# Optimization experiments

Hardware: AMD Instinct MI355X
Metric: run time of the kernel (lower is better)

## Reference

```python
import jax, jax.numpy as jnp
import numpy as np

N = 50000      # nodes
E = 800000     # edges (before self loops)
IN = 128       # in_channels
H = 4          # heads
C = 32         # hidden_channels (per head)
D = H * C      # concat output dim = 128
NEG_SLOPE = 0.2
LN_EPS = 1e-5


def setup_inputs() -> dict:
    key = jax.random.key(0)
    ks = jax.random.split(key, 24)
    def p(k, shape, s=0.1):
        return jax.random.normal(k, shape, dtype=jnp.float32) * s
    inp = {
        "x": p(ks[0], (N, IN), 1.0),
        "edge_index": jax.random.randint(ks[1], (2, E), 0, N, dtype=jnp.int32),
    }
    i = 2
    for l, ind in [(0, IN), (1, D)]:
        inp[f"Wl{l}"] = p(ks[i], (ind, D)); i += 1
        inp[f"bl{l}"] = p(ks[i], (D,), 0.02); i += 1
        inp[f"Wr{l}"] = p(ks[i], (ind, D)); i += 1
        inp[f"br{l}"] = p(ks[i], (D,), 0.02); i += 1
        inp[f"att{l}"] = p(ks[i], (H, C)); i += 1
        inp[f"Wres{l}"] = p(ks[i], (ind, D)); i += 1
        inp[f"bias{l}"] = p(ks[i], (D,), 0.02); i += 1
        inp[f"g{l}"] = jnp.ones((D,), jnp.float32)
        inp[f"be{l}"] = jnp.zeros((D,), jnp.float32)
    return inp


def _gatv2_layer(x, src, dst, Wl, bl, Wr, br, att, Wres, bias):
    """GATv2Conv with concat heads, add_self_loops already applied, residual."""
    n = x.shape[0]
    xl = (x @ Wl + bl).reshape(n, H, C)   # source transform
    xr = (x @ Wr + br).reshape(n, H, C)   # target transform
    # edge-level attention logits: e = a . LeakyReLU(xl[j] + xr[i])  [E, H]
    eh = jax.nn.leaky_relu(xl[src] + xr[dst], negative_slope=NEG_SLOPE)  # [E,H,C]
    score = jnp.einsum('ehc,hc->eh', eh, att)                            # [E,H]
    # segment softmax over incoming edges of each destination node
    smax = jax.ops.segment_max(score, dst, num_segments=n)               # [N,H]
    ex = jnp.exp(score - smax[dst])
    ssum = jax.ops.segment_sum(ex, dst, num_segments=n)                  # [N,H]
    alpha = ex / ssum[dst]                                               # [E,H]
    msg = xl[src] * alpha[:, :, None]                                    # [E,H,C]
    out = jax.ops.segment_sum(msg, dst, num_segments=n).reshape(n, D)
    return out + x @ Wres + bias  # residual (bias=False linear) + final bias


def _layernorm_relu(x, g, b):
    mu = jnp.mean(x, axis=-1, keepdims=True)
    var = jnp.mean(jnp.square(x - mu), axis=-1, keepdims=True)
    return jax.nn.relu((x - mu) * jax.lax.rsqrt(var + LN_EPS) * g + b)


def reference(x, edge_index,
              Wl0, bl0, Wr0, br0, att0, Wres0, bias0, g0, be0,
              Wl1, bl1, Wr1, br1, att1, Wres1, bias1, g1, be1):
    n = x.shape[0]
    loops = jnp.arange(n, dtype=edge_index.dtype)
    src = jnp.concatenate([edge_index[0], loops])  # add_self_loops=True
    dst = jnp.concatenate([edge_index[1], loops])
    h = _gatv2_layer(x, src, dst, Wl0, bl0, Wr0, br0, att0, Wres0, bias0)
    h = _layernorm_relu(h, g0, be0)
    h = _gatv2_layer(h, src, dst, Wl1, bl1, Wr1, br1, att1, Wres1, bias1)
    h = _layernorm_relu(h, g1, be1)
    return h
```

## Files before the change

kernel.cpp:

```cpp
#include <hip/hip_runtime.h>
#include <math.h>

#define D 128
#define LRELU 0.2f
#define LN_EPS 1e-5f
#define INV_LN2 1.4426950408889634f

#define NBMAX 512
#define CAP 4096
#define P1CHUNK 8192

typedef __attribute__((ext_vector_type(8))) short short8;
typedef __attribute__((ext_vector_type(8))) unsigned short ushort8;
typedef __attribute__((ext_vector_type(4))) float f32x4;
typedef __attribute__((ext_vector_type(2))) float f32x2;
typedef __attribute__((ext_vector_type(2))) unsigned int u32x2;
typedef __attribute__((ext_vector_type(4))) unsigned int u32x4;

static __device__ __forceinline__ unsigned short f2bf(float f) {
    union { float f; unsigned u; } a; a.f = f;
    unsigned r = a.u + 0x7FFFu + ((a.u >> 16) & 1u);
    return (unsigned short)(r >> 16);
}

static __device__ __forceinline__ f32x2 pk_add(f32x2 a, f32x2 b) {
    f32x2 d; asm("v_pk_add_f32 %0, %1, %2" : "=v"(d) : "v"(a), "v"(b)); return d;
}
static __device__ __forceinline__ f32x2 pk_mul(f32x2 a, f32x2 b) {
    f32x2 d; asm("v_pk_mul_f32 %0, %1, %2" : "=v"(d) : "v"(a), "v"(b)); return d;
}
static __device__ __forceinline__ f32x2 pk_fma(f32x2 a, f32x2 b, f32x2 c) {
    f32x2 d; asm("v_pk_fma_f32 %0, %1, %2, %3" : "=v"(d) : "v"(a), "v"(b), "v"(c)); return d;
}
static __device__ __forceinline__ f32x2 pk_abs(f32x2 a) {
    u32x2 u = __builtin_bit_cast(u32x2, a);
    u &= 0x7FFFFFFFu;
    return __builtin_bit_cast(f32x2, u);
}
static __device__ __forceinline__ f32x2 bf2x(unsigned u) {
    f32x2 r;
    r.x = __uint_as_float(u << 16);
    r.y = __uint_as_float(u & 0xFFFF0000u);
    return r;
}

static __device__ __forceinline__ float red4_dpp(float p) {
    int v = __builtin_amdgcn_update_dpp(0, __builtin_bit_cast(int, p), 0xB1, 0xf, 0xf, true);
    p += __builtin_bit_cast(float, v);
    v = __builtin_amdgcn_update_dpp(0, __builtin_bit_cast(int, p), 0x4E, 0xf, 0xf, true);
    p += __builtin_bit_cast(float, v);
    return p;
}

#define SCB 256


__global__ __launch_bounds__(256) void k_prep(
    const int* __restrict__ srcp, const int* __restrict__ dstp,
    int* __restrict__ bcur, unsigned* __restrict__ ebuf, int E, int N,
    const float* __restrict__ X, ushort* __restrict__ Xb, int Mp,
    const float* __restrict__ W0, const float* __restrict__ W1, const float* __restrict__ W2,
    const float* __restrict__ W3, const float* __restrict__ W4, const float* __restrict__ W5,
    ushort* __restrict__ Wp, int nP1, int nCV)
{
    const int bx = blockIdx.x;
    const int tid = threadIdx.x;
    if (bx < nP1) {
        __shared__ int h[NBMAX];
        const int E2 = E + N;
        const int e0 = bx * P1CHUNK;
        const int e1 = min(e0 + P1CHUNK, E2);
        for (int t = tid; t < NBMAX; t += 256) h[t] = 0;
        __syncthreads();
        for (int e = e0 + tid; e < e1; e += 256) {
            int d = (e < E) ? dstp[e] : e - E;
            atomicAdd(&h[d >> 7], 1);
        }
        __syncthreads();
        for (int b = tid; b < NBMAX; b += 256) {
            int c = h[b];
            h[b] = c ? atomicAdd(&bcur[b], c) : 0;
        }
        __syncthreads();
        for (int e = e0 + tid; e < e1; e += 256) {
            int d  = (e < E) ? dstp[e] : e - E;
            int sc = (e < E) ? srcp[e] : e - E;
            int b = d >> 7;
            int pos = atomicAdd(&h[b], 1) & (CAP - 1);
            ebuf[(size_t)b * CAP + pos] = ((unsigned)sc << 7) | (unsigned)(d & 127);
        }
    } else if (bx < nP1 + nCV) {
        int idx = (bx - nP1) * 256 + tid;
        if (idx >= Mp * (D / 4)) return;
        ushort4 o;
        if (idx < N * (D / 4)) {
            float4 v = ((const float4*)X)[idx];
            o.x = f2bf(v.x); o.y = f2bf(v.y); o.z = f2bf(v.z); o.w = f2bf(v.w);
        } else {
            o = make_ushort4(0, 0, 0, 0);
        }
        ((ushort4*)Xb)[idx] = o;
    } else {
        int bid = bx - nP1 - nCV;
        int m = bid >> 6;
        int o = ((bid & 63) << 8) + tid;
        const float* W;
        if (m == 0) W = W0; else if (m == 1) W = W1; else if (m == 2) W = W2;
        else if (m == 3) W = W3; else if (m == 4) W = W4; else W = W5;
        int j  = o & 7;
        int l  = (o >> 3) & 63;
        int ct = (o >> 9) & 7;
        int kc = o >> 12;
        int k   = kc * 32 + ((l >> 4) << 3) + j;
        int col = (ct << 4) + (l & 15);
        Wp[m * 16384 + o] = f2bf(W[k * D + col]);
    }
}


__global__ __launch_bounds__(256) void bhist_kernel(const unsigned* __restrict__ ebuf,
                                                    const int* __restrict__ bcur,
                                                    int* __restrict__ deg,
                                                    int* __restrict__ btot, int N) {
    const int b = blockIdx.x;
    const int base = b << 7;
    const int tid = threadIdx.x;
    __shared__ int h[128];
    __shared__ int t2[2];
    if (tid < 128) h[tid] = 0;
    __syncthreads();
    const int cnt = min(bcur[b], CAP);
    for (int k = tid; k < cnt; k += 256) {
        unsigned v = ebuf[(size_t)b * CAP + k];
        atomicAdd(&h[v & 127], 1);
    }
    __syncthreads();
    int v = (tid < 128) ? h[tid] : 0;
    if (tid < 128 && base + tid < N) deg[base + tid] = v;
    #pragma unroll
    for (int o = 32; o >= 1; o >>= 1) v += __shfl_xor(v, o);
    if (tid == 0)  t2[0] = v;
    if (tid == 64) t2[1] = v;
    __syncthreads();
    if (tid == 0) btot[b] = t2[0] + t2[1];
}


static __device__ __forceinline__ void gemm_body(
    int bxg, int seg, int tid,
    const ushort* __restrict__ Xb, const ushort* __restrict__ Wp,
    const float* __restrict__ bl, const float* __restrict__ br,
    ushort* __restrict__ XLb, ushort* __restrict__ XRb, float* __restrict__ RES)
{
    const int l = tid & 63;
    const int wave = tid >> 6;
    const int wr = wave >> 1, wc = wave & 1;
    const int brow = bxg * 128 + wr * 64;
    const ushort* W = Wp + seg * 16384;

    f32x4 acc[4][4] = {};
    const int arow = brow + (l & 15);
    const int koff = (l >> 4) * 8;

    #pragma unroll
    for (int kc = 0; kc < 4; ++kc) {
        short8 A[4], B[4];
        #pragma unroll
        for (int at = 0; at < 4; ++at)
            A[at] = *(const short8*)&Xb[(size_t)(arow + at * 16) * D + kc * 32 + koff];
        #pragma unroll
        for (int ct = 0; ct < 4; ++ct) {
            int ctg = wc * 4 + ct;
            B[ct] = *(const short8*)&W[(((kc * 8 + ctg) * 64) + l) * 8];
        }
        #pragma unroll
        for (int at = 0; at < 4; ++at)
            #pragma unroll
            for (int ct = 0; ct < 4; ++ct)
                acc[at][ct] = __builtin_amdgcn_mfma_f32_16x16x32_bf16(A[at], B[ct], acc[at][ct], 0, 0, 0);
    }

    const int c = l & 15;
    const int r0 = (l >> 4) * 4;
    const float* bias = (seg == 0) ? bl : ((seg == 1) ? br : nullptr);
    #pragma unroll
    for (int ct = 0; ct < 4; ++ct) {
        int gcol = wc * 64 + ct * 16 + c;
        float bv = bias ? bias[gcol] : 0.f;
        #pragma unroll
        for (int at = 0; at < 4; ++at) {
            #pragma unroll
            for (int r = 0; r < 4; ++r) {
                int grow = brow + at * 16 + r0 + r;
                float v = acc[at][ct][r] + bv;
                size_t off = (size_t)grow * D + gcol;
                if (seg == 0)      XLb[off] = f2bf(v);
                else if (seg == 1) XRb[off] = f2bf(v);
                else               RES[off] = v;
            }
        }
    }
}


__global__ __launch_bounds__(256) void k_mid(
    const unsigned* __restrict__ ebuf, const int* __restrict__ bcur,
    const int* __restrict__ deg, const int* __restrict__ btot,
    int* __restrict__ off, int* __restrict__ csrc, int N, int NB, int nblk,
    const ushort* __restrict__ Xb, const ushort* __restrict__ Wp,
    const float* __restrict__ bl, const float* __restrict__ br,
    ushort* __restrict__ XLb, ushort* __restrict__ XRb, float* __restrict__ RES)
{
    const int bx = blockIdx.x;
    if (bx < NB) {
        const int b = bx;
        const int base = b << 7;
        const int tid = threadIdx.x;
        __shared__ int cur[128];
        __shared__ int wsum[4];
        __shared__ int wtot[2];

        int acc = 0;
        for (int t = tid; t < b; t += 256) acc += btot[t];
        #pragma unroll
        for (int o = 32; o >= 1; o >>= 1) acc += __shfl_xor(acc, o);
        if ((tid & 63) == 0) wsum[tid >> 6] = acc;
        __syncthreads();
        const int B = wsum[0] + wsum[1] + wsum[2] + wsum[3];

        int dv = 0;
        if (tid < 128 && base + tid < N) dv = deg[base + tid];
        int incl = dv;
        if (tid < 128) {
            #pragma unroll
            for (int o = 1; o < 64; o <<= 1) {
                int u = __shfl_up(incl, o);
                if ((tid & 63) >= o) incl += u;
            }
        }
        if (tid == 63)  wtot[0] = incl;
        if (tid == 127) wtot[1] = incl;
        __syncthreads();
        if (tid < 128) {
            int add = (tid >= 64) ? wtot[0] : 0;
            int excl = B + add + incl - dv;
            cur[tid] = excl;
            if (base + tid < N) off[base + tid] = excl;
        }
        if (b == NB - 1 && tid == 0) off[N] = B + wtot[0] + wtot[1];
        __syncthreads();

        const int cnt = min(bcur[b], CAP);
        for (int k = tid; k < cnt; k += 256) {
            unsigned v = ebuf[(size_t)b * CAP + k];
            int p = atomicAdd(&cur[v & 127], 1);
            csrc[p] = v >> 7;
        }
    } else {
        int bid = bx - NB;
        int seg = bid / nblk;
        int bxg = bid - seg * nblk;
        gemm_body(bxg, seg, threadIdx.x, Xb, Wp, bl, br, XLb, XRb, RES);
    }
}

__global__ __launch_bounds__(256) void gemm_mfma(
    const ushort* __restrict__ Xb, const ushort* __restrict__ Wp,
    const float* __restrict__ bl, const float* __restrict__ br,
    ushort* __restrict__ XLb, ushort* __restrict__ XRb, float* __restrict__ RES)
{
    gemm_body(blockIdx.x, blockIdx.y, threadIdx.x, Xb, Wp, bl, br, XLb, XRb, RES);
}


__global__ __launch_bounds__(256) void gat_node(
    const ushort* __restrict__ XLb, const ushort* __restrict__ XRb, const float* __restrict__ RES,
    const float* __restrict__ att, const float* __restrict__ bias,
    const float* __restrict__ g, const float* __restrict__ be,
    const int* __restrict__ off, const int* __restrict__ csrc,
    float* __restrict__ OUTf, ushort* __restrict__ OUTb)
{
    const int l = threadIdx.x & 63;
    const int i = blockIdx.x * 16 + (threadIdx.x >> 6) * 4 + (l >> 4);
    const int f = (l & 15) * 8;
    const unsigned ibase = ((unsigned)i << 7) + f;
    const int lb = l & 48;

    f32x2 at06[4], at04[4];
    #pragma unroll
    for (int k = 0; k < 4; ++k) {
        float2 a = *(const float2*)&att[f + k * 2];
        f32x2 av; av.x = a.x; av.y = a.y;
        at06[k] = av * (0.6f * INV_LN2);
        at04[k] = av * (0.4f * INV_LN2);
    }

    u32x4 xru = __builtin_nontemporal_load((const u32x4*)&XRb[ibase]);
    f32x2 xr2[4];
    xr2[0] = bf2x(xru.x); xr2[1] = bf2x(xru.y); xr2[2] = bf2x(xru.z); xr2[3] = bf2x(xru.w);

    const int e0 = off[i], e1 = off[i + 1];
    const int len = e1 - e0;
    int mx = max(len, __shfl_xor(len, 16));
    mx = max(mx, __shfl_xor(mx, 32));

    float m = -1e30f, s = 0.f;
    f32x2 a2[4] = {};

    for (int c0 = 0; c0 < mx; c0 += 16) {
        int myj = __builtin_nontemporal_load(&csrc[min(e0 + c0 + (l & 15), e1 - 1)]);
        const int rem = mx - c0;
        const int nbb = min(4, (rem + 3) >> 2);
        const int kleft = len - c0;

        u32x4 u_[4];
        {
            int s0 = __shfl(myj, lb + 0);
            int s1 = __shfl(myj, lb + 1);
            int s2 = __shfl(myj, lb + 2);
            int s3 = __shfl(myj, lb + 3);
            u_[0] = *(const u32x4*)&XLb[((unsigned)s0 << 7) + f];
            u_[1] = *(const u32x4*)&XLb[((unsigned)s1 << 7) + f];
            u_[2] = *(const u32x4*)&XLb[((unsigned)s2 << 7) + f];
            u_[3] = *(const u32x4*)&XLb[((unsigned)s3 << 7) + f];
        }

        #pragma unroll
        for (int bb = 0; bb < 4; ++bb) {
            if (bb >= nbb) break;
            u32x4 uc[4];
            #pragma unroll
            for (int j = 0; j < 4; ++j) uc[j] = u_[j];
            if (bb + 1 < nbb) {
                int s0 = __shfl(myj, lb + (bb + 1) * 4 + 0);
                int s1 = __shfl(myj, lb + (bb + 1) * 4 + 1);
                int s2 = __shfl(myj, lb + (bb + 1) * 4 + 2);
                int s3 = __shfl(myj, lb + (bb + 1) * 4 + 3);
                u_[0] = *(const u32x4*)&XLb[((unsigned)s0 << 7) + f];
                u_[1] = *(const u32x4*)&XLb[((unsigned)s1 << 7) + f];
                u_[2] = *(const u32x4*)&XLb[((unsigned)s2 << 7) + f];
                u_[3] = *(const u32x4*)&XLb[((unsigned)s3 << 7) + f];
            }

            const int kb = kleft - bb * 4;
            f32x2 xp[4][4];
            float p[4];
            #pragma unroll
            for (int j = 0; j < 4; ++j) {
                xp[j][0] = bf2x(uc[j].x);
                xp[j][1] = bf2x(uc[j].y);
                xp[j][2] = bf2x(uc[j].z);
                xp[j][3] = bf2x(uc[j].w);
                f32x2 v0 = pk_add(xp[j][0], xr2[0]);
                f32x2 pj2 = pk_mul(v0, at06[0]);
                pj2 = pk_fma(pk_abs(v0), at04[0], pj2);
                #pragma unroll
                for (int k = 1; k < 4; ++k) {
                    f32x2 v = pk_add(xp[j][k], xr2[k]);
                    pj2 = pk_fma(v, at06[k], pj2);
                    pj2 = pk_fma(pk_abs(v), at04[k], pj2);
                }
                float pj = pj2.x + pj2.y;
                pj = red4_dpp(pj);
                p[j] = (j < kb) ? pj : -1e30f;
            }
            float pmax = fmaxf(fmaxf(p[0], p[1]), fmaxf(p[2], p[3]));
            float nm = fmaxf(m, pmax);
            float so = exp2f(m - nm);
            float w0 = exp2f(p[0] - nm), w1 = exp2f(p[1] - nm);
            float w2 = exp2f(p[2] - nm), w3 = exp2f(p[3] - nm);
            s = s * so + ((w0 + w1) + (w2 + w3));
            f32x2 so2; so2.x = so; so2.y = so;
            f32x2 w02; w02.x = w0; w02.y = w0;
            f32x2 w12; w12.x = w1; w12.y = w1;
            f32x2 w22; w22.x = w2; w22.y = w2;
            f32x2 w32; w32.x = w3; w32.y = w3;
            #pragma unroll
            for (int k = 0; k < 4; ++k) {
                f32x2 t = pk_mul(xp[0][k], w02);
                t = pk_fma(xp[1][k], w12, t);
                t = pk_fma(xp[2][k], w22, t);
                t = pk_fma(xp[3][k], w32, t);
                a2[k] = pk_fma(a2[k], so2, t);
            }
            m = nm;
        }
    }

    const f32x4 rsA = __builtin_nontemporal_load((const f32x4*)&RES[ibase]);
    const f32x4 rsB = __builtin_nontemporal_load((const f32x4*)&RES[ibase + 4]);
    const float4 biA = *(const float4*)&bias[f];
    const float4 biB = *(const float4*)&bias[f + 4];
    float inv = 1.f / s;
    float r0 = a2[0].x * inv + rsA.x + biA.x;
    float r1 = a2[0].y * inv + rsA.y + biA.y;
    float r2 = a2[1].x * inv + rsA.z + biA.z;
    float r3 = a2[1].y * inv + rsA.w + biA.w;
    float r4 = a2[2].x * inv + rsB.x + biB.x;
    float r5 = a2[2].y * inv + rsB.y + biB.y;
    float r6 = a2[3].x * inv + rsB.z + biB.z;
    float r7 = a2[3].y * inv + rsB.w + biB.w;

    float sum = ((r0 + r1) + (r2 + r3)) + ((r4 + r5) + (r6 + r7));
    float sq  = ((r0 * r0 + r1 * r1) + (r2 * r2 + r3 * r3))
              + ((r4 * r4 + r5 * r5) + (r6 * r6 + r7 * r7));
    #pragma unroll
    for (int o = 8; o >= 1; o >>= 1) {
        sum += __shfl_xor(sum, o);
        sq  += __shfl_xor(sq, o);
    }
    float mu  = sum * (1.f / 128.f);
    float var = sq * (1.f / 128.f) - mu * mu;
    float isd = rsqrtf(var + LN_EPS);
    const float4 gvA = *(const float4*)&g[f];
    const float4 gvB = *(const float4*)&g[f + 4];
    const float4 bvA = *(const float4*)&be[f];
    const float4 bvB = *(const float4*)&be[f + 4];
    float o0 = fmaxf((r0 - mu) * isd * gvA.x + bvA.x, 0.f);
    float o1 = fmaxf((r1 - mu) * isd * gvA.y + bvA.y, 0.f);
    float o2 = fmaxf((r2 - mu) * isd * gvA.z + bvA.z, 0.f);
    float o3 = fmaxf((r3 - mu) * isd * gvA.w + bvA.w, 0.f);
    float o4 = fmaxf((r4 - mu) * isd * gvB.x + bvB.x, 0.f);
    float o5 = fmaxf((r5 - mu) * isd * gvB.y + bvB.y, 0.f);
    float o6 = fmaxf((r6 - mu) * isd * gvB.z + bvB.z, 0.f);
    float o7 = fmaxf((r7 - mu) * isd * gvB.w + bvB.w, 0.f);

    if (OUTb) {
        ushort8 ob;
        ob[0] = f2bf(o0); ob[1] = f2bf(o1); ob[2] = f2bf(o2); ob[3] = f2bf(o3);
        ob[4] = f2bf(o4); ob[5] = f2bf(o5); ob[6] = f2bf(o6); ob[7] = f2bf(o7);
        __builtin_nontemporal_store(ob, (ushort8*)&OUTb[ibase]);
    } else {
        f32x4 oA; oA.x = o0; oA.y = o1; oA.z = o2; oA.w = o3;
        f32x4 oB; oB.x = o4; oB.y = o5; oB.z = o6; oB.w = o7;
        __builtin_nontemporal_store(oA, (f32x4*)&OUTf[ibase]);
        __builtin_nontemporal_store(oB, (f32x4*)&OUTf[ibase + 4]);
    }
}


extern "C" void kernel_launch(void* const* d_in, const int* in_sizes, int n_in,
                              void* d_out, int out_size, void* d_ws, size_t ws_size,
                              hipStream_t stream)
{
    const float* x    = (const float*)d_in[0];
    const int*   ei   = (const int*)d_in[1];
    const float* Wl0  = (const float*)d_in[2];
    const float* bl0  = (const float*)d_in[3];
    const float* Wr0  = (const float*)d_in[4];
    const float* br0  = (const float*)d_in[5];
    const float* att0 = (const float*)d_in[6];
    const float* Wres0= (const float*)d_in[7];
    const float* bias0= (const float*)d_in[8];
    const float* g0   = (const float*)d_in[9];
    const float* be0  = (const float*)d_in[10];
    const float* Wl1  = (const float*)d_in[11];
    const float* bl1  = (const float*)d_in[12];
    const float* Wr1  = (const float*)d_in[13];
    const float* br1  = (const float*)d_in[14];
    const float* att1 = (const float*)d_in[15];
    const float* Wres1= (const float*)d_in[16];
    const float* bias1= (const float*)d_in[17];
    const float* g1   = (const float*)d_in[18];
    const float* be1  = (const float*)d_in[19];

    const int N  = in_sizes[0] / D;
    const int E  = in_sizes[1] / 2;
    const int E2 = E + N;
    const int nblk = (N + 127) / 128;
    const int Mp = nblk * 128;
    const int NB = nblk;

    char* w = (char*)d_ws;
    ushort* Xb  = (ushort*)w; w += (size_t)Mp * D * 2;
    ushort* Hb  = (ushort*)w; w += (size_t)Mp * D * 2;
    ushort* XLb = (ushort*)w; w += (size_t)Mp * D * 2;
    ushort* XRb = (ushort*)w; w += (size_t)Mp * D * 2;
    float*  RES = (float*)w;  w += (size_t)Mp * D * 4;
    ushort* Wp  = (ushort*)w; w += (size_t)6 * 16384 * 2;
    int* deg     = (int*)w; w += (size_t)N * 4;
    int* off     = (int*)w; w += (size_t)(N + 1) * 4;
    int* bcur    = (int*)w; w += (size_t)NBMAX * 4;
    int* btot    = (int*)w; w += (size_t)NBMAX * 4;
    unsigned* ebuf = (unsigned*)w; w += (size_t)NB * CAP * 4;
    int* csrc    = (int*)w; w += (size_t)E2 * 4;

    const int* srcp = ei;
    const int* dstp = ei + E;

    const int nP1 = (E2 + P1CHUNK - 1) / P1CHUNK;
    const int nCV = (Mp * (D / 4) + 255) / 256;
    const int nPW = 6 * 64;
    const int nGM = nblk * 3;

    hipMemsetAsync(bcur, 0, (size_t)NBMAX * 4, stream);
    k_prep<<<nP1 + nCV + nPW, 256, 0, stream>>>(srcp, dstp, bcur, ebuf, E, N,
                                                x, Xb, Mp,
                                                Wl0, Wr0, Wres0, Wl1, Wr1, Wres1,
                                                Wp, nP1, nCV);
    bhist_kernel<<<NB, 256, 0, stream>>>(ebuf, bcur, deg, btot, N);

    k_mid<<<NB + nGM, 256, 0, stream>>>(ebuf, bcur, deg, btot, off, csrc, N, NB, nblk,
                                        Xb, Wp, bl0, br0, XLb, XRb, RES);

    const int gatg = N / 16;
    dim3 ggrid(nblk, 3);

    gat_node<<<gatg, 256, 0, stream>>>(XLb, XRb, RES, att0, bias0, g0, be0, off, csrc, nullptr, Hb);
    gemm_mfma<<<ggrid, 256, 0, stream>>>(Hb, Wp + 3 * 16384, bl1, br1, XLb, XRb, RES);
    gat_node<<<gatg, 256, 0, stream>>>(XLb, XRb, RES, att1, bias1, g1, be1, off, csrc, (float*)d_out, nullptr);
}
```

Before: 186.4 us.

## Store residual in bf16 and split online softmax into two accumulator chains

The residual projection output is now written and read as bf16 instead of fp32, halving that buffer's write and read traffic in the GEMM and node kernels. The gat_node edge loop keeps two independent online-softmax states (max, sum, accumulators) that alternate per sub-batch and are merged at the end. This shortens the serial dependency through the rescale chain so more work can overlap. Weights past the valid count are now explicitly zeroed. The cost is extra registers, a branch per sub-batch, and lower precision in the residual term.

After: 185.1 us. About the same (-0.6%).

```diff
diff --git a/kernel.cpp b/kernel.cpp
--- a/kernel.cpp
+++ b/kernel.cpp
@@ -150,7 +150,7 @@
     int bxg, int seg, int tid,
     const ushort* __restrict__ Xb, const ushort* __restrict__ Wp,
     const float* __restrict__ bl, const float* __restrict__ br,
-    ushort* __restrict__ XLb, ushort* __restrict__ XRb, float* __restrict__ RES)
+    ushort* __restrict__ XLb, ushort* __restrict__ XRb, ushort* __restrict__ RESb)
 {
     const int l = tid & 63;
     const int wave = tid >> 6;
@@ -194,9 +194,9 @@
                 int grow = brow + at * 16 + r0 + r;
                 float v = acc[at][ct][r] + bv;
                 size_t off = (size_t)grow * D + gcol;
-                if (seg == 0)      XLb[off] = f2bf(v);
-                else if (seg == 1) XRb[off] = f2bf(v);
-                else               RES[off] = v;
+                if (seg == 0)      XLb[off]  = f2bf(v);
+                else if (seg == 1) XRb[off]  = f2bf(v);
+                else               RESb[off] = f2bf(v);
             }
         }
     }
@@ -209,7 +209,7 @@
     int* __restrict__ off, int* __restrict__ csrc, int N, int NB, int nblk,
     const ushort* __restrict__ Xb, const ushort* __restrict__ Wp,
     const float* __restrict__ bl, const float* __restrict__ br,
-    ushort* __restrict__ XLb, ushort* __restrict__ XRb, float* __restrict__ RES)
+    ushort* __restrict__ XLb, ushort* __restrict__ XRb, ushort* __restrict__ RESb)
 {
     const int bx = blockIdx.x;
     if (bx < NB) {
@@ -260,21 +260,21 @@
         int bid = bx - NB;
         int seg = bid / nblk;
         int bxg = bid - seg * nblk;
-        gemm_body(bxg, seg, threadIdx.x, Xb, Wp, bl, br, XLb, XRb, RES);
+        gemm_body(bxg, seg, threadIdx.x, Xb, Wp, bl, br, XLb, XRb, RESb);
     }
 }
 
 __global__ __launch_bounds__(256) void gemm_mfma(
     const ushort* __restrict__ Xb, const ushort* __restrict__ Wp,
     const float* __restrict__ bl, const float* __restrict__ br,
-    ushort* __restrict__ XLb, ushort* __restrict__ XRb, float* __restrict__ RES)
+    ushort* __restrict__ XLb, ushort* __restrict__ XRb, ushort* __restrict__ RESb)
 {
-    gemm_body(blockIdx.x, blockIdx.y, threadIdx.x, Xb, Wp, bl, br, XLb, XRb, RES);
+    gemm_body(blockIdx.x, blockIdx.y, threadIdx.x, Xb, Wp, bl, br, XLb, XRb, RESb);
 }
 
 
 __global__ __launch_bounds__(256) void gat_node(
-    const ushort* __restrict__ XLb, const ushort* __restrict__ XRb, const float* __restrict__ RES,
+    const ushort* __restrict__ XLb, const ushort* __restrict__ XRb, const ushort* __restrict__ RESb,
     const float* __restrict__ att, const float* __restrict__ bias,
     const float* __restrict__ g, const float* __restrict__ be,
     const int* __restrict__ off, const int* __restrict__ csrc,
@@ -304,8 +304,10 @@
     int mx = max(len, __shfl_xor(len, 16));
     mx = max(mx, __shfl_xor(mx, 32));
 
-    float m = -1e30f, s = 0.f;
-    f32x2 a2[4] = {};
+    float mA = -1e30f, sA = 0.f;
+    float mB = -1e30f, sB = 0.f;
+    f32x2 aA[4] = {};
+    f32x2 aB[4] = {};
 
     for (int c0 = 0; c0 < mx; c0 += 16) {
         int myj = __builtin_nontemporal_load(&csrc[min(e0 + c0 + (l & 15), e1 - 1)]);
@@ -364,42 +366,72 @@
                 pj = red4_dpp(pj);
                 p[j] = (j < kb) ? pj : -1e30f;
             }
+            float m0 = (bb & 1) ? mB : mA;
+            float s0v = (bb & 1) ? sB : sA;
             float pmax = fmaxf(fmaxf(p[0], p[1]), fmaxf(p[2], p[3]));
-            float nm = fmaxf(m, pmax);
-            float so = exp2f(m - nm);
+            float nm = fmaxf(m0, pmax);
+            float so = exp2f(m0 - nm);
             float w0 = exp2f(p[0] - nm), w1 = exp2f(p[1] - nm);
             float w2 = exp2f(p[2] - nm), w3 = exp2f(p[3] - nm);
-            s = s * so + ((w0 + w1) + (w2 + w3));
+            w0 = (0 < kb) ? w0 : 0.f;
+            w1 = (1 < kb) ? w1 : 0.f;
+            w2 = (2 < kb) ? w2 : 0.f;
+            w3 = (3 < kb) ? w3 : 0.f;
+            float sn = s0v * so + ((w0 + w1) + (w2 + w3));
             f32x2 so2; so2.x = so; so2.y = so;
             f32x2 w02; w02.x = w0; w02.y = w0;
             f32x2 w12; w12.x = w1; w12.y = w1;
             f32x2 w22; w22.x = w2; w22.y = w2;
             f32x2 w32; w32.x = w3; w32.y = w3;
-            #pragma unroll
-            for (int k = 0; k < 4; ++k) {
-                f32x2 t = pk_mul(xp[0][k], w02);
-                t = pk_fma(xp[1][k], w12, t);
-                t = pk_fma(xp[2][k], w22, t);
-                t = pk_fma(xp[3][k], w32, t);
-                a2[k] = pk_fma(a2[k], so2, t);
+            if (bb & 1) {
+                #pragma unroll
+                for (int k = 0; k < 4; ++k) {
+                    f32x2 t = pk_mul(xp[0][k], w02);
+                    t = pk_fma(xp[1][k], w12, t);
+                    t = pk_fma(xp[2][k], w22, t);
+                    t = pk_fma(xp[3][k], w32, t);
+                    aB[k] = pk_fma(aB[k], so2, t);
+                }
+                mB = nm; sB = sn;
+            } else {
+                #pragma unroll
+                for (int k = 0; k < 4; ++k) {
+                    f32x2 t = pk_mul(xp[0][k], w02);
+                    t = pk_fma(xp[1][k], w12, t);
+                    t = pk_fma(xp[2][k], w22, t);
+                    t = pk_fma(xp[3][k], w32, t);
+                    aA[k] = pk_fma(aA[k], so2, t);
+                }
+                mA = nm; sA = sn;
             }
-            m = nm;
-        }
-    }
-
-    const f32x4 rsA = __builtin_nontemporal_load((const f32x4*)&RES[ibase]);
-    const f32x4 rsB = __builtin_nontemporal_load((const f32x4*)&RES[ibase + 4]);
+        }
+    }
+
+    float nmv = fmaxf(mA, mB);
+    float soA = exp2f(mA - nmv);
+    float soB = exp2f(mB - nmv);
+    float s = sA * soA + sB * soB;
+    f32x2 soA2; soA2.x = soA; soA2.y = soA;
+    f32x2 soB2; soB2.x = soB; soB2.y = soB;
+    f32x2 a2[4];
+    #pragma unroll
+    for (int k = 0; k < 4; ++k)
+        a2[k] = pk_add(pk_mul(aA[k], soA2), pk_mul(aB[k], soB2));
+
+    u32x4 ru = __builtin_nontemporal_load((const u32x4*)&RESb[ibase]);
+    f32x2 rs2[4];
+    rs2[0] = bf2x(ru.x); rs2[1] = bf2x(ru.y); rs2[2] = bf2x(ru.z); rs2[3] = bf2x(ru.w);
     const float4 biA = *(const float4*)&bias[f];
     const float4 biB = *(const float4*)&bias[f + 4];
     float inv = 1.f / s;
-    float r0 = a2[0].x * inv + rsA.x + biA.x;
-    float r1 = a2[0].y * inv + rsA.y + biA.y;
-    float r2 = a2[1].x * inv + rsA.z + biA.z;
-    float r3 = a2[1].y * inv + rsA.w + biA.w;
-    float r4 = a2[2].x * inv + rsB.x + biB.x;
-    float r5 = a2[2].y * inv + rsB.y + biB.y;
-    float r6 = a2[3].x * inv + rsB.z + biB.z;
-    float r7 = a2[3].y * inv + rsB.w + biB.w;
+    float r0 = a2[0].x * inv + rs2[0].x + biA.x;
+    float r1 = a2[0].y * inv + rs2[0].y + biA.y;
+    float r2 = a2[1].x * inv + rs2[1].x + biA.z;
+    float r3 = a2[1].y * inv + rs2[1].y + biA.w;
+    float r4 = a2[2].x * inv + rs2[2].x + biB.x;
+    float r5 = a2[2].y * inv + rs2[2].y + biB.y;
+    float r6 = a2[3].x * inv + rs2[3].x + biB.z;
+    float r7 = a2[3].y * inv + rs2[3].y + biB.w;
 
     float sum = ((r0 + r1) + (r2 + r3)) + ((r4 + r5) + (r6 + r7));
     float sq  = ((r0 * r0 + r1 * r1) + (r2 * r2 + r3 * r3))
@@ -472,12 +504,12 @@
     const int NB = nblk;
 
     char* w = (char*)d_ws;
-    ushort* Xb  = (ushort*)w; w += (size_t)Mp * D * 2;
-    ushort* Hb  = (ushort*)w; w += (size_t)Mp * D * 2;
-    ushort* XLb = (ushort*)w; w += (size_t)Mp * D * 2;
-    ushort* XRb = (ushort*)w; w += (size_t)Mp * D * 2;
-    float*  RES = (float*)w;  w += (size_t)Mp * D * 4;
-    ushort* Wp  = (ushort*)w; w += (size_t)6 * 16384 * 2;
+    ushort* Xb   = (ushort*)w; w += (size_t)Mp * D * 2;
+    ushort* Hb   = (ushort*)w; w += (size_t)Mp * D * 2;
+    ushort* XLb  = (ushort*)w; w += (size_t)Mp * D * 2;
+    ushort* XRb  = (ushort*)w; w += (size_t)Mp * D * 2;
+    ushort* RESb = (ushort*)w; w += (size_t)Mp * D * 2;
+    ushort* Wp   = (ushort*)w; w += (size_t)6 * 16384 * 2;
     int* deg     = (int*)w; w += (size_t)N * 4;
     int* off     = (int*)w; w += (size_t)(N + 1) * 4;
     int* bcur    = (int*)w; w += (size_t)NBMAX * 4;
@@ -501,12 +533,12 @@
     bhist_kernel<<<NB, 256, 0, stream>>>(ebuf, bcur, deg, btot, N);
 
     k_mid<<<NB + nGM, 256, 0, stream>>>(ebuf, bcur, deg, btot, off, csrc, N, NB, nblk,
-                                        Xb, Wp, bl0, br0, XLb, XRb, RES);
+                                        Xb, Wp, bl0, br0, XLb, XRb, RESb);
 
     const int gatg = N / 16;
     dim3 ggrid(nblk, 3);
 
-    gat_node<<<gatg, 256, 0, stream>>>(XLb, XRb, RES, att0, bias0, g0, be0, off, csrc, nullptr, Hb);
-    gemm_mfma<<<ggrid, 256, 0, stream>>>(Hb, Wp + 3 * 16384, bl1, br1, XLb, XRb, RES);
-    gat_node<<<gatg, 256, 0, stream>>>(XLb, XRb, RES, att1, bias1, g1, be1, off, csrc, (float*)d_out, nullptr);
-}
+    gat_node<<<gatg, 256, 0, stream>>>(XLb, XRb, RESb, att0, bias0, g0, be0, off, csrc, nullptr, Hb);
+    gemm_mfma<<<ggrid, 256, 0, stream>>>(Hb, Wp + 3 * 16384, bl1, br1, XLb, XRb, RESb);
+    gat_node<<<gatg, 256, 0, stream>>>(XLb, XRb, RESb, att1, bias1, g1, be1, off, csrc, (float*)d_out, nullptr);
+}
```
